# Kernel tuning notes

Hardware: AMD Instinct MI355X
Metric: run time of the kernel (lower is better)

Reference implementation:

```python
import jax, jax.numpy as jnp
import numpy as np

B, CIN, IMG = 2, 3, 128
E, NH, WS, L, HID = 256, 8, 8, 4, 1024
HD = E // NH
SCALE = HD ** -0.5
T = WS * WS  # tokens per window


def _layernorm(x, g, b):
    m = x.mean(-1, keepdims=True)
    v = ((x - m) ** 2).mean(-1, keepdims=True)
    return (x - m) * jax.lax.rsqrt(v + 1e-5) * g + b


def _build_mask(H, W, ws, ss):
    # Swin shifted-window mask, built with static numpy (H,W,ws,ss are static)
    img = np.zeros((H, W), np.float32)
    cnt = 0
    sl = lambda n: (slice(0, n - ws), slice(n - ws, n - ss), slice(n - ss, n))
    for h in sl(H):
        for w in sl(W):
            img[h, w] = cnt
            cnt += 1
    mw = img.reshape(H // ws, ws, W // ws, ws).transpose(0, 2, 1, 3).reshape(-1, ws * ws)
    d = mw[:, None, :] - mw[:, :, None]
    return jnp.asarray(np.where(d != 0, -100.0, 0.0).astype(np.float32))  # [nW,T,T]


def _win_attn(xseq, H, W, wqkv, bqkv, wproj, bproj, mask):
    Bn, N, C = xseq.shape
    nWh, nWw = H // WS, W // WS
    nW = nWh * nWw
    # window partition: [B,N,C] -> [B*nW, T, C]
    xw = xseq.reshape(Bn, nWh, WS, nWw, WS, C).transpose(0, 1, 3, 2, 4, 5).reshape(Bn * nW, T, C)
    qkv = (xw @ wqkv + bqkv).reshape(Bn * nW, T, 3, NH, HD).transpose(2, 0, 3, 1, 4)
    q, k, v = qkv[0], qkv[1], qkv[2]  # [B*nW, NH, T, HD]
    attn = jnp.einsum('whtd,whsd->whts', q, k) * SCALE
    if mask is not None:
        attn = (attn.reshape(Bn, nW, NH, T, T) + mask[None, :, None]).reshape(Bn * nW, NH, T, T)
    attn = jax.nn.softmax(attn, axis=-1)
    out = jnp.einsum('whts,whsd->wthd', attn, v).reshape(Bn * nW, T, C)
    out = out @ wproj + bproj
    # window merge
    out = out.reshape(Bn, nWh, nWw, WS, WS, C).transpose(0, 1, 3, 2, 4, 5).reshape(Bn, H * W, C)
    return out


def _forward(x, in_w, in_b, pos, ln1_g, ln1_b, qkv_w, qkv_b, proj_w, proj_b,
             ln2_g, ln2_b, mlp_w1, mlp_b1, mlp_w2, mlp_b2, out_w, out_b):
    Bx, _, H, W = x.shape
    ss = WS // 2
    y = jnp.einsum('bchw,ec->behw', x, in_w) + in_b[None, :, None, None] + pos
    seq = y.transpose(0, 2, 3, 1).reshape(Bx, H * W, E)
    mask = _build_mask(H, W, WS, ss)
    for i in range(L):
        shifted = (i % 2 == 1)
        if shifted:
            seq = jnp.roll(seq.reshape(Bx, H, W, E), (-ss, -ss), (1, 2)).reshape(Bx, H * W, E)
        h = _layernorm(seq, ln1_g[i], ln1_b[i])
        seq = seq + _win_attn(h, H, W, qkv_w[i], qkv_b[i], proj_w[i], proj_b[i],
                              mask if shifted else None)
        h = _layernorm(seq, ln2_g[i], ln2_b[i])
        seq = seq + (jax.nn.gelu(h @ mlp_w1[i] + mlp_b1[i], approximate=False) @ mlp_w2[i] + mlp_b2[i])
        if shifted:
            seq = jnp.roll(seq.reshape(Bx, H, W, E), (ss, ss), (1, 2)).reshape(Bx, H * W, E)
    out = seq.reshape(Bx, H, W, E).transpose(0, 3, 1, 2)
    return jnp.einsum('bchw,ec->behw', out, out_w) + out_b[None, :, None, None]


def setup_inputs() -> dict:
    key = jax.random.key(0)
    ks = jax.random.split(key, 10)
    std = jnp.float32(0.02)
    return {
        'x': jax.random.normal(ks[0], (B, CIN, IMG, IMG), jnp.float32),
        'in_w': jax.random.normal(ks[1], (E, CIN), jnp.float32) * std,
        'in_b': jnp.zeros((E,), jnp.float32),
        'pos': jax.random.normal(ks[2], (1, E, IMG, IMG), jnp.float32) * std,
        'ln1_g': jnp.ones((L, E), jnp.float32),
        'ln1_b': jnp.zeros((L, E), jnp.float32),
        'qkv_w': jax.random.normal(ks[3], (L, E, 3 * E), jnp.float32) * std,
        'qkv_b': jnp.zeros((L, 3 * E), jnp.float32),
        'proj_w': jax.random.normal(ks[4], (L, E, E), jnp.float32) * std,
        'proj_b': jnp.zeros((L, E), jnp.float32),
        'ln2_g': jnp.ones((L, E), jnp.float32),
        'ln2_b': jnp.zeros((L, E), jnp.float32),
        'mlp_w1': jax.random.normal(ks[5], (L, E, HID), jnp.float32) * std,
        'mlp_b1': jnp.zeros((L, HID), jnp.float32),
        'mlp_w2': jax.random.normal(ks[6], (L, HID, E), jnp.float32) * std,
        'mlp_b2': jnp.zeros((L, E), jnp.float32),
        'out_w': jax.random.normal(ks[7], (E, E), jnp.float32) * std,
        'out_b': jnp.zeros((E,), jnp.float32),
    }


def reference(x, in_w, in_b, pos, ln1_g, ln1_b, qkv_w, qkv_b, proj_w, proj_b,
              ln2_g, ln2_b, mlp_w1, mlp_b1, mlp_w2, mlp_b2, out_w, out_b):
    return _forward(x, in_w, in_b, pos, ln1_g, ln1_b, qkv_w, qkv_b, proj_w, proj_b,
                    ln2_g, ln2_b, mlp_w1, mlp_b1, mlp_w2, mlp_b2, out_w, out_b)
```

## Files before the change

### kernel.cpp

```cpp
#include <hip/hip_runtime.h>
#include <hip/hip_bf16.h>
#include <math.h>

#define E_DIM 256
#define NPB 16384
#define M_TOT 32768

typedef __attribute__((ext_vector_type(4))) float f32x4;
typedef __attribute__((ext_vector_type(8))) short s16x8;

__device__ inline unsigned short f2bu(float f) {
  __hip_bfloat16 h = __float2bfloat16(f);
  return *reinterpret_cast<unsigned short*>(&h);
}
__device__ inline float bu2f(unsigned short u) {
  union { unsigned int i; float f; } x; x.i = ((unsigned int)u) << 16; return x.f;
}
__device__ inline void gload16(const void* g, void* l) {
  __builtin_amdgcn_global_load_lds(
      (const __attribute__((address_space(1))) void*)g,
      (__attribute__((address_space(3))) void*)l, 16, 0, 0);
}
__device__ inline float fgelu(float v) {
  float u2 = 2.0f * v * (0.7978845608f + 0.0356774081f * v * v);
  u2 = fminf(u2, 30.0f);
  float e = __expf(u2);
  return v * (e / (e + 1.0f));
}

__global__ __launch_bounds__(256) void wconv_all(
    const float* __restrict__ qkv_w, const float* __restrict__ proj_w,
    const float* __restrict__ w1,    const float* __restrict__ w2,
    const float* __restrict__ outw,
    unsigned short* __restrict__ qkvT, unsigned short* __restrict__ projT,
    unsigned short* __restrict__ w1T,  unsigned short* __restrict__ w2T,
    unsigned short* __restrict__ outwb)
{
  int bid = blockIdx.x;
  if (bid >= 3072) {
    int idx = (bid - 3072) * 1024 + threadIdx.x * 4;
    float4 v = *(const float4*)(outw + idx);
    ushort4 u; u.x = f2bu(v.x); u.y = f2bu(v.y); u.z = f2bu(v.z); u.w = f2bu(v.w);
    *(ushort4*)(outwb + idx) = u;
    return;
  }
  int layer = bid / 768, r = bid % 768;
  const float* W; unsigned short* Wt; int K, N, txt, tile;
  if (r < 192)      { W = qkv_w  + (size_t)layer*196608; Wt = qkvT + (size_t)layer*196608; K=256;  N=768;  txt=24; tile=r; }
  else if (r < 256) { W = proj_w + (size_t)layer*65536;  Wt = projT+ (size_t)layer*65536;  K=256;  N=256;  txt=8;  tile=r-192; }
  else if (r < 512) { W = w1     + (size_t)layer*262144; Wt = w1T  + (size_t)layer*262144; K=256;  N=1024; txt=32; tile=r-256; }
  else              { W = w2     + (size_t)layer*262144; Wt = w2T  + (size_t)layer*262144; K=1024; N=256;  txt=8;  tile=r-512; }
  int nb = (tile % txt) * 32, kb = (tile / txt) * 32;
  __shared__ float t[32][33];
  int tx = threadIdx.x & 31, ty = threadIdx.x >> 5;
  #pragma unroll
  for (int i = 0; i < 32; i += 8)
    t[ty + i][tx] = W[(size_t)(kb + ty + i) * N + nb + tx];
  __syncthreads();
  #pragma unroll
  for (int i = 0; i < 32; i += 8)
    Wt[(size_t)(nb + ty + i) * K + kb + tx] = f2bu(t[tx][ty + i]);
}

__global__ __launch_bounds__(256) void embed_ln(
    const float* __restrict__ x, const float* __restrict__ in_w,
    const float* __restrict__ in_b, const float* __restrict__ pos,
    const float* __restrict__ g, const float* __restrict__ bta,
    float* __restrict__ seq, unsigned short* __restrict__ hb)
{
  __shared__ float ld[32][33];
  __shared__ float vbuf[32][260];
  __shared__ float2 st[32];
  const int n0 = blockIdx.x * 32;
  const int b = n0 >> 14, np = n0 & (NPB - 1);
  const int tx = threadIdx.x & 31, ty = threadIdx.x >> 5;

  float x0[4], x1[4], x2[4], sp[4] = {0,0,0,0}, qp[4] = {0,0,0,0};
  #pragma unroll
  for (int i = 0; i < 4; i++) {
    int n = np + ty + 8*i;
    x0[i] = x[(b*3 + 0)*NPB + n];
    x1[i] = x[(b*3 + 1)*NPB + n];
    x2[i] = x[(b*3 + 2)*NPB + n];
  }
  for (int ec = 0; ec < 8; ec++) {
    int e0 = ec * 32;
    #pragma unroll
    for (int i = 0; i < 4; i++)
      ld[ty + 8*i][tx] = pos[(size_t)(e0 + ty + 8*i) * NPB + np + tx];
    __syncthreads();
    #pragma unroll
    for (int i = 0; i < 4; i++) {
      int e = e0 + tx;
      float v = x0[i]*in_w[e*3+0] + x1[i]*in_w[e*3+1] + x2[i]*in_w[e*3+2]
              + in_b[e] + ld[tx][ty + 8*i];
      vbuf[ty + 8*i][e] = v;
      sp[i] += v; qp[i] += v * v;
    }
    __syncthreads();
  }
  #pragma unroll
  for (int i = 0; i < 4; i++) {
    #pragma unroll
    for (int off = 1; off < 32; off <<= 1) {
      sp[i] += __shfl_xor(sp[i], off);
      qp[i] += __shfl_xor(qp[i], off);
    }
    if (tx == 0) st[ty + 8*i] = (float2){sp[i], qp[i]};
  }
  __syncthreads();
  const int token = threadIdx.x >> 3, ch = threadIdx.x & 7;
  float2 sq = st[token];
  float mean = sq.x * (1.0f / 256.0f);
  float rstd = rsqrtf(sq.y * (1.0f / 256.0f) - mean * mean + 1e-5f);
  float* srow = seq + (size_t)(n0 + token) * 256;
  unsigned short* hrow = hb + (size_t)(n0 + token) * 256;
  #pragma unroll
  for (int u = 0; u < 8; u++) {
    int e = ch * 32 + u * 4;
    float4 v = *(float4*)&vbuf[token][e];
    *(float4*)(srow + e) = v;
    float4 gg = *(const float4*)(g + e);
    float4 bb = *(const float4*)(bta + e);
    ushort4 h;
    h.x = f2bu((v.x - mean) * rstd * gg.x + bb.x);
    h.y = f2bu((v.y - mean) * rstd * gg.y + bb.y);
    h.z = f2bu((v.z - mean) * rstd * gg.z + bb.z);
    h.w = f2bu((v.w - mean) * rstd * gg.w + bb.w);
    *(ushort4*)(hrow + e) = h;
  }
}

__device__ inline int rowf(int r) { return (r & 3) ^ ((r >> 2) & 3); }

template<int ACT, int OCHW, int OBF>
__global__ __launch_bounds__(512) void mgemm_a(
    const unsigned short* __restrict__ A, const unsigned short* __restrict__ Wt,
    const float* __restrict__ bias, void* __restrict__ Cv, int N, int K)
{
  __shared__ unsigned short Al[2][128 * 32];
  __shared__ unsigned short Bl[2][256 * 32];
  const int tid  = threadIdx.x;
  const int lane = tid & 63;
  const int wid  = tid >> 6;
  const int wr = wid >> 2, wc = wid & 3;
  const int nbx = N >> 8;
  const int bid = blockIdx.x;
  const int lt  = (bid & 7) * ((int)gridDim.x >> 3) + (bid >> 3);
  const int bn  = (lt % nbx) * 256, bm = (lt / nbx) * 128;

  f32x4 acc[4][4];
  #pragma unroll
  for (int m = 0; m < 4; m++)
    #pragma unroll
    for (int n = 0; n < 4; n++)
      acc[m][n] = (f32x4){0.f, 0.f, 0.f, 0.f};

  const int srow = tid >> 2;
  const int cs   = (tid & 3) ^ rowf(srow);
  const unsigned short* aSrc  = A  + (size_t)(bm + srow) * K + cs * 8;
  const unsigned short* bSrc0 = Wt + (size_t)(bn + srow) * K + cs * 8;
  const unsigned short* bSrc1 = Wt + (size_t)(bn + srow + 128) * K + cs * 8;

  const int slotx = (lane >> 4) ^ (lane & 3) ^ ((lane >> 2) & 3);
  const int aoff = (wr*64 + (lane & 15)) * 64 + slotx * 16;
  const int boff = (wc*64 + (lane & 15)) * 64 + slotx * 16;

  {
    gload16(aSrc,  (char*)Al[0] + tid * 16);
    gload16(bSrc0, (char*)Bl[0] + tid * 16);
    gload16(bSrc1, (char*)Bl[0] + tid * 16 + 8192);
  }
  __syncthreads();

  const int nt = K >> 5;
  int cur = 0;
  for (int t = 0; t < nt; ++t) {
    if (t + 1 < nt) {
      int k0 = (t + 1) << 5;
      gload16(aSrc + k0,  (char*)Al[cur ^ 1] + tid * 16);
      gload16(bSrc0 + k0, (char*)Bl[cur ^ 1] + tid * 16);
      gload16(bSrc1 + k0, (char*)Bl[cur ^ 1] + tid * 16 + 8192);
    }
    const char* ab = (const char*)Al[cur] + aoff;
    const char* bb = (const char*)Bl[cur] + boff;
    s16x8 af[4], bf_[4];
    #pragma unroll
    for (int m = 0; m < 4; m++) af[m]  = *(const s16x8*)(ab + m * 1024);
    #pragma unroll
    for (int n = 0; n < 4; n++) bf_[n] = *(const s16x8*)(bb + n * 1024);
    #pragma unroll
    for (int m = 0; m < 4; m++)
      #pragma unroll
      for (int n = 0; n < 4; n++)
        acc[m][n] = __builtin_amdgcn_mfma_f32_16x16x32_bf16(af[m], bf_[n], acc[m][n], 0, 0, 0);
    __syncthreads();
    cur ^= 1;
  }

  float bv[4];
  #pragma unroll
  for (int n = 0; n < 4; n++) bv[n] = bias[bn + wc*64 + n*16 + (lane & 15)];

  #pragma unroll
  for (int m = 0; m < 4; m++) {
    int row0 = bm + wr*64 + m*16 + (lane >> 4) * 4;
    #pragma unroll
    for (int n = 0; n < 4; n++) {
      int col = bn + wc*64 + n*16 + (lane & 15);
      if (OCHW) {
        int bb2 = row0 >> 14, n0 = row0 & (NPB - 1);
        float4 st;
        st.x = acc[m][n][0] + bv[n]; st.y = acc[m][n][1] + bv[n];
        st.z = acc[m][n][2] + bv[n]; st.w = acc[m][n][3] + bv[n];
        *(float4*)((float*)Cv + (size_t)bb2 * E_DIM * NPB + (size_t)col * NPB + n0) = st;
      } else {
        #pragma unroll
        for (int j = 0; j < 4; j++) {
          int row = row0 + j;
          float v = acc[m][n][j] + bv[n];
          if (ACT) v = fgelu(v);
          if (OBF) ((unsigned short*)Cv)[(size_t)row * N + col] = f2bu(v);
          else     ((float*)Cv)[(size_t)row * N + col] = v;
        }
      }
    }
  }
}

template<int LNC>
__global__ __launch_bounds__(512) void mgemm_res(
    const unsigned short* __restrict__ A, const unsigned short* __restrict__ Wt,
    const float* __restrict__ bias, float* __restrict__ seq,
    const float* __restrict__ gamma, const float* __restrict__ beta,
    unsigned short* __restrict__ hb, int K)
{
  __shared__ unsigned short Al[2][64 * 32];
  __shared__ unsigned short Bl[2][256 * 32];
  __shared__ float2 ws[64][4];
  const int tid  = threadIdx.x;
  const int lane = tid & 63;
  const int wid  = tid >> 6;
  const int wr = wid >> 2, wc = wid & 3;
  const int bid = blockIdx.x;
  const int lt  = (bid & 7) * ((int)gridDim.x >> 3) + (bid >> 3);
  const int bm  = lt * 64;

  f32x4 acc[2][4];
  #pragma unroll
  for (int m = 0; m < 2; m++)
    #pragma unroll
    for (int n = 0; n < 4; n++)
      acc[m][n] = (f32x4){0.f, 0.f, 0.f, 0.f};

  const int srow = tid >> 2;
  const int cs   = (tid & 3) ^ rowf(srow);
  const unsigned short* aSrc  = A  + (size_t)(bm + srow) * K + cs * 8;
  const unsigned short* bSrc0 = Wt + (size_t)srow * K + cs * 8;
  const unsigned short* bSrc1 = Wt + (size_t)(srow + 128) * K + cs * 8;

  const int slotx = (lane >> 4) ^ (lane & 3) ^ ((lane >> 2) & 3);
  const int aoff = (wr*32 + (lane & 15)) * 64 + slotx * 16;
  const int boff = (wc*64 + (lane & 15)) * 64 + slotx * 16;

  {
    if (tid < 256) gload16(aSrc, (char*)Al[0] + tid * 16);
    gload16(bSrc0, (char*)Bl[0] + tid * 16);
    gload16(bSrc1, (char*)Bl[0] + tid * 16 + 8192);
  }
  __syncthreads();

  const int nt = K >> 5;
  int cur = 0;
  for (int t = 0; t < nt; ++t) {
    if (t + 1 < nt) {
      int k0 = (t + 1) << 5;
      if (tid < 256) gload16(aSrc + k0, (char*)Al[cur ^ 1] + tid * 16);
      gload16(bSrc0 + k0, (char*)Bl[cur ^ 1] + tid * 16);
      gload16(bSrc1 + k0, (char*)Bl[cur ^ 1] + tid * 16 + 8192);
    }
    const char* ab = (const char*)Al[cur] + aoff;
    const char* bb = (const char*)Bl[cur] + boff;
    s16x8 af[2], bf_[4];
    #pragma unroll
    for (int m = 0; m < 2; m++) af[m]  = *(const s16x8*)(ab + m * 1024);
    #pragma unroll
    for (int n = 0; n < 4; n++) bf_[n] = *(const s16x8*)(bb + n * 1024);
    #pragma unroll
    for (int m = 0; m < 2; m++)
      #pragma unroll
      for (int n = 0; n < 4; n++)
        acc[m][n] = __builtin_amdgcn_mfma_f32_16x16x32_bf16(af[m], bf_[n], acc[m][n], 0, 0, 0);
    __syncthreads();
    cur ^= 1;
  }

  const int lc = lane & 15, lg = lane >> 4;
  float bv[4], gv[4], btv[4];
  #pragma unroll
  for (int n = 0; n < 4; n++) {
    int col = wc*64 + n*16 + lc;
    bv[n] = bias[col];
    if (LNC) { gv[n] = gamma[col]; btv[n] = beta[col]; }
  }

  #pragma unroll
  for (int m = 0; m < 2; m++)
    #pragma unroll
    for (int j = 0; j < 4; j++) {
      int row = bm + wr*32 + m*16 + lg*4 + j;
      #pragma unroll
      for (int n = 0; n < 4; n++) {
        int col = wc*64 + n*16 + lc;
        float v = acc[m][n][j] + bv[n] + seq[(size_t)row * 256 + col];
        seq[(size_t)row * 256 + col] = v;
        acc[m][n][j] = v;
      }
    }

  if (LNC) {
    #pragma unroll
    for (int m = 0; m < 2; m++)
      #pragma unroll
      for (int j = 0; j < 4; j++) {
        float s = acc[m][0][j] + acc[m][1][j] + acc[m][2][j] + acc[m][3][j];
        float q = acc[m][0][j]*acc[m][0][j] + acc[m][1][j]*acc[m][1][j]
                + acc[m][2][j]*acc[m][2][j] + acc[m][3][j]*acc[m][3][j];
        s += __shfl_xor(s, 1); q += __shfl_xor(q, 1);
        s += __shfl_xor(s, 2); q += __shfl_xor(q, 2);
        s += __shfl_xor(s, 4); q += __shfl_xor(q, 4);
        s += __shfl_xor(s, 8); q += __shfl_xor(q, 8);
        if (lc == 0) ws[wr*32 + m*16 + lg*4 + j][wc] = (float2){s, q};
      }
    __syncthreads();
  }

  #pragma unroll
  for (int m = 0; m < 2; m++)
    #pragma unroll
    for (int j = 0; j < 4; j++) {
      int r = wr*32 + m*16 + lg*4 + j;
      float mean = 0.f, rstd = 1.f;
      if (LNC) {
        float2 a0 = ws[r][0], a1 = ws[r][1], a2 = ws[r][2], a3 = ws[r][3];
        float s = a0.x + a1.x + a2.x + a3.x;
        float q = a0.y + a1.y + a2.y + a3.y;
        mean = s * (1.0f / 256.0f);
        rstd = rsqrtf(q * (1.0f / 256.0f) - mean * mean + 1e-5f);
      }
      unsigned short* hrow = hb + (size_t)(bm + r) * 256;
      #pragma unroll
      for (int n = 0; n < 4; n++) {
        int col = wc*64 + n*16 + lc;
        float o = LNC ? (acc[m][n][j] - mean) * rstd * gv[n] + btv[n]
                      : acc[m][n][j];
        hrow[col] = f2bu(o);
      }
    }
}

template<int SHIFT>
__global__ __launch_bounds__(256) void mattn(
    const unsigned short* __restrict__ qkv, unsigned short* __restrict__ out)
{
  __shared__ unsigned short Vt_s[4][32 * 64];
  __shared__ unsigned short Pl_s[4][64 * 64];
  const int tid = threadIdx.x, wid = tid >> 6, l = tid & 63;
  const int task = blockIdx.x * 4 + wid;
  const int head = task & 7;
  const int wf = task >> 3;
  const int b = wf >> 8, win = wf & 255;
  const int wh = win >> 4, ww = win & 15;
  unsigned short* Vt = Vt_s[wid];
  unsigned short* Pl = Pl_s[wid];
  const int lg = l >> 4, lc = l & 15;

  auto tok_of = [&](int t) -> int {
    int hs = wh * 8 + (t >> 3), ws = ww * 8 + (t & 7);
    if (SHIFT) { hs = (hs + 4) & 127; ws = (ws + 4) & 127; }
    return b * NPB + hs * 128 + ws;
  };
  auto reg_of = [&](int t) -> int {
    int hs = wh * 8 + (t >> 3), ws = ww * 8 + (t & 7);
    int a = (hs < 120) ? 0 : ((hs < 124) ? 1 : 2);
    int c = (ws < 120) ? 0 : ((ws < 124) ? 1 : 2);
    return a * 3 + c;
  };

  s16x8 qf[4], kf[4];
  #pragma unroll
  for (int m = 0; m < 4; m++) {
    const unsigned short* rp = qkv + (size_t)tok_of(m * 16 + lc) * 768 + head * 32 + lg * 8;
    qf[m] = *(const s16x8*)(rp);
    kf[m] = *(const s16x8*)(rp + 256);
  }
  {
    const unsigned short* vp = qkv + (size_t)tok_of(l) * 768 + 512 + head * 32;
    #pragma unroll
    for (int d8 = 0; d8 < 4; d8++) {
      s16x8 vv = *(const s16x8*)(vp + d8 * 8);
      #pragma unroll
      for (int j = 0; j < 8; j++) {
        int d = d8 * 8 + j;
        Vt[(d * 64 + l) ^ ((d & 7) << 3)] = (unsigned short)vv[j];
      }
    }
  }

  f32x4 sT[4][4];
  #pragma unroll
  for (int m = 0; m < 4; m++)
    #pragma unroll
    for (int qt = 0; qt < 4; qt++) {
      f32x4 z = (f32x4){0.f, 0.f, 0.f, 0.f};
      sT[m][qt] = __builtin_amdgcn_mfma_f32_16x16x32_bf16(kf[m], qf[qt], z, 0, 0, 0);
    }

  int qreg[4], kreg2[16];
  if (SHIFT) {
    #pragma unroll
    for (int qt = 0; qt < 4; qt++) qreg[qt] = reg_of(qt * 16 + lc);
    #pragma unroll
    for (int m = 0; m < 4; m++)
      #pragma unroll
      for (int r = 0; r < 4; r++) kreg2[m * 4 + r] = reg_of(m * 16 + lg * 4 + r);
  }

  const float scale = 0.17677669529663687f;
  #pragma unroll
  for (int qt = 0; qt < 4; qt++) {
    float mx = -1e30f;
    #pragma unroll
    for (int m = 0; m < 4; m++)
      #pragma unroll
      for (int r = 0; r < 4; r++) {
        float s = sT[m][qt][r] * scale;
        if (SHIFT && qreg[qt] != kreg2[m * 4 + r]) s -= 100.0f;
        sT[m][qt][r] = s;
        mx = fmaxf(mx, s);
      }
    mx = fmaxf(mx, __shfl_xor(mx, 16));
    mx = fmaxf(mx, __shfl_xor(mx, 32));
    float sum = 0.f;
    #pragma unroll
    for (int m = 0; m < 4; m++)
      #pragma unroll
      for (int r = 0; r < 4; r++) {
        float p = __expf(sT[m][qt][r] - mx);
        sT[m][qt][r] = p;
        sum += p;
      }
    sum += __shfl_xor(sum, 16);
    sum += __shfl_xor(sum, 32);
    float inv = 1.0f / sum;
    int q = qt * 16 + lc;
    #pragma unroll
    for (int m = 0; m < 4; m++) {
      ushort4 pk;
      pk.x = f2bu(sT[m][qt][0] * inv);
      pk.y = f2bu(sT[m][qt][1] * inv);
      pk.z = f2bu(sT[m][qt][2] * inv);
      pk.w = f2bu(sT[m][qt][3] * inv);
      *(ushort4*)(Pl + ((q * 64 + m * 16 + lg * 4) ^ ((q & 7) << 3))) = pk;
    }
  }

  f32x4 oacc[4][2];
  #pragma unroll
  for (int qt = 0; qt < 4; qt++)
    #pragma unroll
    for (int n = 0; n < 2; n++)
      oacc[qt][n] = (f32x4){0.f, 0.f, 0.f, 0.f};
  #pragma unroll
  for (int kb = 0; kb < 2; kb++) {
    s16x8 pa[4], vb[2];
    #pragma unroll
    for (int qt = 0; qt < 4; qt++) {
      int q = qt * 16 + lc;
      pa[qt] = *(const s16x8*)(Pl + ((q * 64 + kb * 32 + lg * 8) ^ ((q & 7) << 3)));
    }
    #pragma unroll
    for (int n = 0; n < 2; n++) {
      int d = n * 16 + lc;
      vb[n] = *(const s16x8*)(Vt + ((d * 64 + kb * 32 + lg * 8) ^ ((d & 7) << 3)));
    }
    #pragma unroll
    for (int qt = 0; qt < 4; qt++)
      #pragma unroll
      for (int n = 0; n < 2; n++)
        oacc[qt][n] = __builtin_amdgcn_mfma_f32_16x16x32_bf16(pa[qt], vb[n], oacc[qt][n], 0, 0, 0);
  }

  #pragma unroll
  for (int qt = 0; qt < 4; qt++)
    #pragma unroll
    for (int r = 0; r < 4; r++) {
      int q = qt * 16 + lg * 4 + r;
      unsigned short* ob = out + (size_t)tok_of(q) * 256 + head * 32;
      ob[lc]      = f2bu(oacc[qt][0][r]);
      ob[16 + lc] = f2bu(oacc[qt][1][r]);
    }
}

extern "C" void kernel_launch(void* const* d_in, const int* in_sizes, int n_in,
                              void* d_out, int out_size, void* d_ws, size_t ws_size,
                              hipStream_t stream) {
  (void)in_sizes; (void)n_in; (void)out_size; (void)ws_size;
  const float* x      = (const float*)d_in[0];
  const float* in_w   = (const float*)d_in[1];
  const float* in_b   = (const float*)d_in[2];
  const float* pos    = (const float*)d_in[3];
  const float* ln1_g  = (const float*)d_in[4];
  const float* ln1_b  = (const float*)d_in[5];
  const float* qkv_w  = (const float*)d_in[6];
  const float* qkv_b  = (const float*)d_in[7];
  const float* proj_w = (const float*)d_in[8];
  const float* proj_b = (const float*)d_in[9];
  const float* ln2_g  = (const float*)d_in[10];
  const float* ln2_b  = (const float*)d_in[11];
  const float* mlp_w1 = (const float*)d_in[12];
  const float* mlp_b1 = (const float*)d_in[13];
  const float* mlp_w2 = (const float*)d_in[14];
  const float* mlp_b2 = (const float*)d_in[15];
  const float* out_w  = (const float*)d_in[16];
  const float* out_b  = (const float*)d_in[17];
  float* outp = (float*)d_out;

  char* p = (char*)d_ws;
  float* seq = (float*)p;                 p += (size_t)M_TOT * E_DIM * 4;
  unsigned short* bigb = (unsigned short*)p; p += (size_t)M_TOT * 1024 * 2;
  unsigned short* hb = (unsigned short*)p;   p += (size_t)M_TOT * E_DIM * 2;
  unsigned short* wb = (unsigned short*)p;
  unsigned short* qkvT = wb;
  unsigned short* projT = qkvT + 4 * 768 * 256;
  unsigned short* w1T   = projT + 4 * 256 * 256;
  unsigned short* w2T   = w1T   + 4 * 1024 * 256;
  unsigned short* outwb = w2T   + 4 * 256 * 1024;

  wconv_all<<<3136, 256, 0, stream>>>(qkv_w, proj_w, mlp_w1, mlp_w2, out_w,
                                      qkvT, projT, w1T, w2T, outwb);
  embed_ln<<<1024, 256, 0, stream>>>(x, in_w, in_b, pos, ln1_g, ln1_b, seq, hb);

  for (int i = 0; i < 4; i++) {
    int shifted = i & 1;
    mgemm_a<0,0,1><<<768, 512, 0, stream>>>(
        hb, qkvT + (size_t)i*768*256, qkv_b + i*768, bigb, 768, 256);
    if (shifted) mattn<1><<<1024, 256, 0, stream>>>(bigb, hb);
    else         mattn<0><<<1024, 256, 0, stream>>>(bigb, hb);
    mgemm_res<1><<<512, 512, 0, stream>>>(
        hb, projT + (size_t)i*256*256, proj_b + i*256, seq,
        ln2_g + i*256, ln2_b + i*256, hb, 256);
    mgemm_a<1,0,1><<<1024, 512, 0, stream>>>(
        hb, w1T + (size_t)i*1024*256, mlp_b1 + i*1024, bigb, 1024, 256);
    if (i < 3)
      mgemm_res<1><<<512, 512, 0, stream>>>(
          bigb, w2T + (size_t)i*256*1024, mlp_b2 + i*256, seq,
          ln1_g + (i+1)*256, ln1_b + (i+1)*256, hb, 1024);
    else
      mgemm_res<0><<<512, 512, 0, stream>>>(
          bigb, w2T + (size_t)i*256*1024, mlp_b2 + i*256, seq,
          nullptr, nullptr, hb, 1024);
  }

  mgemm_a<0,1,0><<<256, 512, 0, stream>>>(
      hb, outwb, out_b, outp, 256, 256);
}
```

Measured before the change: 613.6 us.

## Fuse QKV projection into per-window attention kernel, dropping the QKV buffer

Adds a kernel that, per window, loads the 64 token rows of the normalized activations into LDS and runs the QKV GEMM with weights streamed from global memory. It keeps Q, K and V in shared memory and then runs masked softmax attention for all 8 heads, one head per wave. This removes the separate QKV GEMM launch and the round trip of the 768-wide QKV intermediate through global memory. In exchange the kernel uses about 128KB of LDS per block, so only one 512-thread block fits per CU across 512 blocks. The attention scale is now folded into Q before it is rounded to bf16, which slightly changes rounding.

```diff
diff --git a/kernel.cpp b/kernel.cpp
--- a/kernel.cpp
+++ b/kernel.cpp
@@ -133,6 +133,222 @@
 
 __device__ inline int rowf(int r) { return (r & 3) ^ ((r >> 2) & 3); }
 
+template<int SHIFT>
+__global__ __launch_bounds__(512) void qkv_attn(
+    const unsigned short* __restrict__ hbuf, const unsigned short* __restrict__ qkvT,
+    const float* __restrict__ qkv_b, unsigned short* __restrict__ hout)
+{
+  __shared__ unsigned short AQ[32768];
+  __shared__ unsigned short Ks[16384];
+  __shared__ unsigned short Vt[16384];
+  const int tid = threadIdx.x, lane = tid & 63, wc = tid >> 6;
+  const int lc = lane & 15, lg = lane >> 4;
+  const int wf = blockIdx.x;
+  const int b = wf >> 8, win = wf & 255;
+  const int wh = win >> 4, ww = win & 15;
+
+  auto tok_of = [&](int t) -> int {
+    int hs = wh * 8 + (t >> 3), ws = ww * 8 + (t & 7);
+    if (SHIFT) { hs = (hs + 4) & 127; ws = (ws + 4) & 127; }
+    return b * NPB + hs * 128 + ws;
+  };
+  auto reg_of = [&](int t) -> int {
+    int hs = wh * 8 + (t >> 3), ws = ww * 8 + (t & 7);
+    int a = (hs < 120) ? 0 : ((hs < 124) ? 1 : 2);
+    int c = (ws < 120) ? 0 : ((ws < 124) ? 1 : 2);
+    return a * 3 + c;
+  };
+
+  #pragma unroll
+  for (int jj = 0; jj < 4; jj++) {
+    int chunk = tid + jj * 512;
+    int r = chunk >> 5, c = chunk & 31;
+    int cg = (c & 24) | ((c & 7) ^ (r & 7));
+    gload16(hbuf + (size_t)tok_of(r) * 256 + cg * 8, (char*)AQ + chunk * 16);
+  }
+  __syncthreads();
+
+  const int fmap0 = 2*wc, fmap1 = 2*wc+1, fmap2 = 16+2*wc, fmap3 = 17+2*wc,
+            fmap4 = 32+2*wc, fmap5 = 33+2*wc;
+  int fmap[6] = {fmap0, fmap1, fmap2, fmap3, fmap4, fmap5};
+  f32x4 acc[4][6];
+  #pragma unroll
+  for (int m = 0; m < 4; m++)
+    #pragma unroll
+    for (int j = 0; j < 6; j++)
+      acc[m][j] = (f32x4){0.f, 0.f, 0.f, 0.f};
+
+  const unsigned short* bb[6];
+  #pragma unroll
+  for (int j = 0; j < 6; j++)
+    bb[j] = qkvT + (size_t)(fmap[j] * 16 + lc) * 256 + lg * 8;
+
+  s16x8 bcur[6];
+  #pragma unroll
+  for (int j = 0; j < 6; j++) bcur[j] = *(const s16x8*)(bb[j]);
+
+  #pragma unroll
+  for (int t = 0; t < 8; t++) {
+    s16x8 bnext[6];
+    if (t < 7) {
+      #pragma unroll
+      for (int j = 0; j < 6; j++) bnext[j] = *(const s16x8*)(bb[j] + (t + 1) * 32);
+    }
+    s16x8 aF[4];
+    #pragma unroll
+    for (int m = 0; m < 4; m++) {
+      int r = m * 16 + lc;
+      int g = t * 4 + lg;
+      int cc = (g & 24) | ((g & 7) ^ (r & 7));
+      aF[m] = *(const s16x8*)(AQ + r * 256 + cc * 8);
+    }
+    #pragma unroll
+    for (int m = 0; m < 4; m++)
+      #pragma unroll
+      for (int j = 0; j < 6; j++)
+        acc[m][j] = __builtin_amdgcn_mfma_f32_16x16x32_bf16(aF[m], bcur[j], acc[m][j], 0, 0, 0);
+    if (t < 7) {
+      #pragma unroll
+      for (int j = 0; j < 6; j++) bcur[j] = bnext[j];
+    }
+  }
+
+  float bv[6];
+  #pragma unroll
+  for (int j = 0; j < 6; j++) bv[j] = qkv_b[fmap[j] * 16 + lc];
+  const float scale = 0.17677669529663687f;
+
+  #pragma unroll
+  for (int j = 0; j < 6; j++) {
+    int col = fmap[j] * 16 + lc;
+    #pragma unroll
+    for (int m = 0; m < 4; m++)
+      #pragma unroll
+      for (int r = 0; r < 4; r++) {
+        int t = m * 16 + lg * 4 + r;
+        float v = acc[m][j][r] + bv[j];
+        if (j < 2) {
+          int qc = col, c = qc >> 3;
+          int cc = (c & 24) | ((c & 7) ^ (t & 7));
+          AQ[16384 + t * 256 + cc * 8 + (qc & 7)] = f2bu(v * scale);
+        } else if (j < 4) {
+          int kc = col - 256, c = kc >> 3;
+          int cc = (c & 24) | ((c & 7) ^ (t & 7));
+          Ks[t * 256 + cc * 8 + (kc & 7)] = f2bu(v);
+        } else {
+          int d = col - 512 - wc * 32;
+          int tc = (t >> 3) ^ (d & 7);
+          Vt[wc * 2048 + d * 64 + tc * 8 + (t & 7)] = f2bu(v);
+        }
+      }
+  }
+
+  s16x8 qf[4], kf[4];
+  #pragma unroll
+  for (int m = 0; m < 4; m++) {
+    int t = m * 16 + lc;
+    int g = wc * 4 + lg;
+    int cc = (g & 24) | ((g & 7) ^ (t & 7));
+    qf[m] = *(const s16x8*)(AQ + 16384 + t * 256 + cc * 8);
+    kf[m] = *(const s16x8*)(Ks + t * 256 + cc * 8);
+  }
+  __syncthreads();
+
+  f32x4 sT[4][4];
+  #pragma unroll
+  for (int m = 0; m < 4; m++)
+    #pragma unroll
+    for (int qt = 0; qt < 4; qt++) {
+      f32x4 z = (f32x4){0.f, 0.f, 0.f, 0.f};
+      sT[m][qt] = __builtin_amdgcn_mfma_f32_16x16x32_bf16(kf[m], qf[qt], z, 0, 0, 0);
+    }
+
+  int qreg[4], kreg2[16];
+  if (SHIFT) {
+    #pragma unroll
+    for (int qt = 0; qt < 4; qt++) qreg[qt] = reg_of(qt * 16 + lc);
+    #pragma unroll
+    for (int m = 0; m < 4; m++)
+      #pragma unroll
+      for (int r = 0; r < 4; r++) kreg2[m * 4 + r] = reg_of(m * 16 + lg * 4 + r);
+  }
+
+  unsigned short* Pl = AQ + wc * 4096;
+  #pragma unroll
+  for (int qt = 0; qt < 4; qt++) {
+    float mx = -1e30f;
+    #pragma unroll
+    for (int m = 0; m < 4; m++)
+      #pragma unroll
+      for (int r = 0; r < 4; r++) {
+        float s = sT[m][qt][r];
+        if (SHIFT && qreg[qt] != kreg2[m * 4 + r]) s -= 100.0f;
+        sT[m][qt][r] = s;
+        mx = fmaxf(mx, s);
+      }
+    mx = fmaxf(mx, __shfl_xor(mx, 16));
+    mx = fmaxf(mx, __shfl_xor(mx, 32));
+    float sum = 0.f;
+    #pragma unroll
+    for (int m = 0; m < 4; m++)
+      #pragma unroll
+      for (int r = 0; r < 4; r++) {
+        float p = __expf(sT[m][qt][r] - mx);
+        sT[m][qt][r] = p;
+        sum += p;
+      }
+    sum += __shfl_xor(sum, 16);
+    sum += __shfl_xor(sum, 32);
+    float inv = 1.0f / sum;
+    int q = qt * 16 + lc;
+    #pragma unroll
+    for (int m = 0; m < 4; m++) {
+      ushort4 pk;
+      pk.x = f2bu(sT[m][qt][0] * inv);
+      pk.y = f2bu(sT[m][qt][1] * inv);
+      pk.z = f2bu(sT[m][qt][2] * inv);
+      pk.w = f2bu(sT[m][qt][3] * inv);
+      *(ushort4*)(Pl + ((q * 64 + m * 16 + lg * 4) ^ ((q & 7) << 3))) = pk;
+    }
+  }
+
+  f32x4 oacc[4][2];
+  #pragma unroll
+  for (int qt = 0; qt < 4; qt++)
+    #pragma unroll
+    for (int n = 0; n < 2; n++)
+      oacc[qt][n] = (f32x4){0.f, 0.f, 0.f, 0.f};
+  #pragma unroll
+  for (int kb = 0; kb < 2; kb++) {
+    s16x8 pa[4], vb[2];
+    #pragma unroll
+    for (int qt = 0; qt < 4; qt++) {
+      int q = qt * 16 + lc;
+      pa[qt] = *(const s16x8*)(Pl + ((q * 64 + kb * 32 + lg * 8) ^ ((q & 7) << 3)));
+    }
+    #pragma unroll
+    for (int n = 0; n < 2; n++) {
+      int d = n * 16 + lc;
+      vb[n] = *(const s16x8*)(Vt + wc * 2048 + d * 64 + (((kb * 4 + lg) ^ (d & 7)) * 8));
+    }
+    #pragma unroll
+    for (int qt = 0; qt < 4; qt++)
+      #pragma unroll
+      for (int n = 0; n < 2; n++)
+        oacc[qt][n] = __builtin_amdgcn_mfma_f32_16x16x32_bf16(pa[qt], vb[n], oacc[qt][n], 0, 0, 0);
+  }
+
+  #pragma unroll
+  for (int qt = 0; qt < 4; qt++)
+    #pragma unroll
+    for (int r = 0; r < 4; r++) {
+      int q = qt * 16 + lg * 4 + r;
+      unsigned short* ob = hout + (size_t)tok_of(q) * 256 + wc * 32;
+      ob[lc]      = f2bu(oacc[qt][0][r]);
+      ob[16 + lc] = f2bu(oacc[qt][1][r]);
+    }
+}
+
 template<int ACT, int OCHW, int OBF>
 __global__ __launch_bounds__(512) void mgemm_a(
     const unsigned short* __restrict__ A, const unsigned short* __restrict__ Wt,
@@ -183,12 +399,12 @@
       gload16(bSrc1 + k0, (char*)Bl[cur ^ 1] + tid * 16 + 8192);
     }
     const char* ab = (const char*)Al[cur] + aoff;
-    const char* bb = (const char*)Bl[cur] + boff;
+    const char* bbp = (const char*)Bl[cur] + boff;
     s16x8 af[4], bf_[4];
     #pragma unroll
     for (int m = 0; m < 4; m++) af[m]  = *(const s16x8*)(ab + m * 1024);
     #pragma unroll
-    for (int n = 0; n < 4; n++) bf_[n] = *(const s16x8*)(bb + n * 1024);
+    for (int n = 0; n < 4; n++) bf_[n] = *(const s16x8*)(bbp + n * 1024);
     #pragma unroll
     for (int m = 0; m < 4; m++)
       #pragma unroll
@@ -280,12 +496,12 @@
       gload16(bSrc1 + k0, (char*)Bl[cur ^ 1] + tid * 16 + 8192);
     }
     const char* ab = (const char*)Al[cur] + aoff;
-    const char* bb = (const char*)Bl[cur] + boff;
+    const char* bbp = (const char*)Bl[cur] + boff;
     s16x8 af[2], bf_[4];
     #pragma unroll
     for (int m = 0; m < 2; m++) af[m]  = *(const s16x8*)(ab + m * 1024);
     #pragma unroll
-    for (int n = 0; n < 4; n++) bf_[n] = *(const s16x8*)(bb + n * 1024);
+    for (int n = 0; n < 4; n++) bf_[n] = *(const s16x8*)(bbp + n * 1024);
     #pragma unroll
     for (int m = 0; m < 2; m++)
       #pragma unroll
@@ -356,149 +572,6 @@
                       : acc[m][n][j];
         hrow[col] = f2bu(o);
       }
-    }
-}
-
-template<int SHIFT>
-__global__ __launch_bounds__(256) void mattn(
-    const unsigned short* __restrict__ qkv, unsigned short* __restrict__ out)
-{
-  __shared__ unsigned short Vt_s[4][32 * 64];
-  __shared__ unsigned short Pl_s[4][64 * 64];
-  const int tid = threadIdx.x, wid = tid >> 6, l = tid & 63;
-  const int task = blockIdx.x * 4 + wid;
-  const int head = task & 7;
-  const int wf = task >> 3;
-  const int b = wf >> 8, win = wf & 255;
-  const int wh = win >> 4, ww = win & 15;
-  unsigned short* Vt = Vt_s[wid];
-  unsigned short* Pl = Pl_s[wid];
-  const int lg = l >> 4, lc = l & 15;
-
-  auto tok_of = [&](int t) -> int {
-    int hs = wh * 8 + (t >> 3), ws = ww * 8 + (t & 7);
-    if (SHIFT) { hs = (hs + 4) & 127; ws = (ws + 4) & 127; }
-    return b * NPB + hs * 128 + ws;
-  };
-  auto reg_of = [&](int t) -> int {
-    int hs = wh * 8 + (t >> 3), ws = ww * 8 + (t & 7);
-    int a = (hs < 120) ? 0 : ((hs < 124) ? 1 : 2);
-    int c = (ws < 120) ? 0 : ((ws < 124) ? 1 : 2);
-    return a * 3 + c;
-  };
-
-  s16x8 qf[4], kf[4];
-  #pragma unroll
-  for (int m = 0; m < 4; m++) {
-    const unsigned short* rp = qkv + (size_t)tok_of(m * 16 + lc) * 768 + head * 32 + lg * 8;
-    qf[m] = *(const s16x8*)(rp);
-    kf[m] = *(const s16x8*)(rp + 256);
-  }
-  {
-    const unsigned short* vp = qkv + (size_t)tok_of(l) * 768 + 512 + head * 32;
-    #pragma unroll
-    for (int d8 = 0; d8 < 4; d8++) {
-      s16x8 vv = *(const s16x8*)(vp + d8 * 8);
-      #pragma unroll
-      for (int j = 0; j < 8; j++) {
-        int d = d8 * 8 + j;
-        Vt[(d * 64 + l) ^ ((d & 7) << 3)] = (unsigned short)vv[j];
-      }
-    }
-  }
-
-  f32x4 sT[4][4];
-  #pragma unroll
-  for (int m = 0; m < 4; m++)
-    #pragma unroll
-    for (int qt = 0; qt < 4; qt++) {
-      f32x4 z = (f32x4){0.f, 0.f, 0.f, 0.f};
-      sT[m][qt] = __builtin_amdgcn_mfma_f32_16x16x32_bf16(kf[m], qf[qt], z, 0, 0, 0);
-    }
-
-  int qreg[4], kreg2[16];
-  if (SHIFT) {
-    #pragma unroll
-    for (int qt = 0; qt < 4; qt++) qreg[qt] = reg_of(qt * 16 + lc);
-    #pragma unroll
-    for (int m = 0; m < 4; m++)
-      #pragma unroll
-      for (int r = 0; r < 4; r++) kreg2[m * 4 + r] = reg_of(m * 16 + lg * 4 + r);
-  }
-
-  const float scale = 0.17677669529663687f;
-  #pragma unroll
-  for (int qt = 0; qt < 4; qt++) {
-    float mx = -1e30f;
-    #pragma unroll
-    for (int m = 0; m < 4; m++)
-      #pragma unroll
-      for (int r = 0; r < 4; r++) {
-        float s = sT[m][qt][r] * scale;
-        if (SHIFT && qreg[qt] != kreg2[m * 4 + r]) s -= 100.0f;
-        sT[m][qt][r] = s;
-        mx = fmaxf(mx, s);
-      }
-    mx = fmaxf(mx, __shfl_xor(mx, 16));
-    mx = fmaxf(mx, __shfl_xor(mx, 32));
-    float sum = 0.f;
-    #pragma unroll
-    for (int m = 0; m < 4; m++)
-      #pragma unroll
-      for (int r = 0; r < 4; r++) {
-        float p = __expf(sT[m][qt][r] - mx);
-        sT[m][qt][r] = p;
-        sum += p;
-      }
-    sum += __shfl_xor(sum, 16);
-    sum += __shfl_xor(sum, 32);
-    float inv = 1.0f / sum;
-    int q = qt * 16 + lc;
-    #pragma unroll
-    for (int m = 0; m < 4; m++) {
-      ushort4 pk;
-      pk.x = f2bu(sT[m][qt][0] * inv);
-      pk.y = f2bu(sT[m][qt][1] * inv);
-      pk.z = f2bu(sT[m][qt][2] * inv);
-      pk.w = f2bu(sT[m][qt][3] * inv);
-      *(ushort4*)(Pl + ((q * 64 + m * 16 + lg * 4) ^ ((q & 7) << 3))) = pk;
-    }
-  }
-
-  f32x4 oacc[4][2];
-  #pragma unroll
-  for (int qt = 0; qt < 4; qt++)
-    #pragma unroll
-    for (int n = 0; n < 2; n++)
-      oacc[qt][n] = (f32x4){0.f, 0.f, 0.f, 0.f};
-  #pragma unroll
-  for (int kb = 0; kb < 2; kb++) {
-    s16x8 pa[4], vb[2];
-    #pragma unroll
-    for (int qt = 0; qt < 4; qt++) {
-      int q = qt * 16 + lc;
-      pa[qt] = *(const s16x8*)(Pl + ((q * 64 + kb * 32 + lg * 8) ^ ((q & 7) << 3)));
-    }
-    #pragma unroll
-    for (int n = 0; n < 2; n++) {
-      int d = n * 16 + lc;
-      vb[n] = *(const s16x8*)(Vt + ((d * 64 + kb * 32 + lg * 8) ^ ((d & 7) << 3)));
-    }
-    #pragma unroll
-    for (int qt = 0; qt < 4; qt++)
-      #pragma unroll
-      for (int n = 0; n < 2; n++)
-        oacc[qt][n] = __builtin_amdgcn_mfma_f32_16x16x32_bf16(pa[qt], vb[n], oacc[qt][n], 0, 0, 0);
-  }
-
-  #pragma unroll
-  for (int qt = 0; qt < 4; qt++)
-    #pragma unroll
-    for (int r = 0; r < 4; r++) {
-      int q = qt * 16 + lg * 4 + r;
-      unsigned short* ob = out + (size_t)tok_of(q) * 256 + head * 32;
-      ob[lc]      = f2bu(oacc[qt][0][r]);
-      ob[16 + lc] = f2bu(oacc[qt][1][r]);
     }
 }
 
@@ -543,10 +616,8 @@
 
   for (int i = 0; i < 4; i++) {
     int shifted = i & 1;
-    mgemm_a<0,0,1><<<768, 512, 0, stream>>>(
-        hb, qkvT + (size_t)i*768*256, qkv_b + i*768, bigb, 768, 256);
-    if (shifted) mattn<1><<<1024, 256, 0, stream>>>(bigb, hb);
-    else         mattn<0><<<1024, 256, 0, stream>>>(bigb, hb);
+    if (shifted) qkv_attn<1><<<512, 512, 0, stream>>>(hb, qkvT + (size_t)i*768*256, qkv_b + i*768, hb);
+    else         qkv_attn<0><<<512, 512, 0, stream>>>(hb, qkvT + (size_t)i*768*256, qkv_b + i*768, hb);
     mgemm_res<1><<<512, 512, 0, stream>>>(
         hb, projT + (size_t)i*256*256, proj_b + i*256, seq,
         ln2_g + i*256, ln2_b + i*256, hb, 256);
```

After: 606.3 us. Within noise of the previous version (-1.2%).
